# Performance work log

Hardware: AMD Instinct MI355X
Metric: run time of the kernel (lower is better)

## Reference

```python
import jax, jax.numpy as jnp
import numpy as np

# 9 jitter shifts: (L, R, T, B) padding applied to `input`; `target` gets the
# opposite padding (L<->R, T<->B swapped), producing a 1-pixel relative shift.
SHIFTS = ((0, 0, 0, 0), (0, 0, 1, 0), (0, 0, 0, 1), (1, 0, 0, 0), (0, 1, 0, 0),
          (1, 0, 1, 0), (0, 1, 0, 1), (0, 1, 1, 0), (1, 0, 0, 1))
SMIN_K = 32.0


def _shifted_diff(inp, tgt, L, R, T, B):
    # get_opposite in the original simply swaps the pad pair
    Lt, Rt = R, L
    Tt, Bt = B, T
    # ConstantPad2d((L,R,T,B)) pads last dim by (L,R), second-to-last by (T,B)
    pi = jnp.pad(inp, ((0, 0), (T, B), (L, R)))
    pt = jnp.pad(tgt, ((0, 0), (Tt, Bt), (Lt, Rt)))  # same padded shape
    d = jnp.abs(pi - pt)
    n, m, k = d.shape
    # crop back to the original (batch, max_len, dim) window
    return d[:, T:m - B, L:k - R]


def setup_inputs() -> dict:
    key = jax.random.key(0)
    k1, k2 = jax.random.split(key)
    B, T, D = 64, 2048, 80
    return {
        "input": jax.random.normal(k1, (B, T, D), dtype=jnp.float32),
        "target": jax.random.normal(k2, (B, T, D), dtype=jnp.float32),
    }


def reference(input, target):
    # (batch, max_len, dim, 9): abs-diff for each of the 9 relative shifts
    diffs = jnp.stack(
        [_shifted_diff(input, target, L, R, T, B) for (L, R, T, B) in SHIFTS],
        axis=-1,
    )
    # smooth minimum over the 9 shifts: -log(sum(exp(-k*t)))/k (stable via logsumexp)
    sm = -jax.scipy.special.logsumexp(-SMIN_K * diffs, axis=-1) / SMIN_K
    center = diffs[..., 0]  # unshifted abs-diff
    # average of the center diff and the smooth-min, reduced to a scalar loss
    return 0.5 * (jnp.mean(center) + jnp.mean(sm))
```

## Files before the change

### kernel.cpp

```cpp
#include <hip/hip_runtime.h>
#include <math.h>

#define BATCH 64
#define TLEN 2048
#define DIM 80
#define DQ (DIM / 4)
#define TT 4
#define TCHUNKS (TLEN / TT)
#define THREADS 256
#define NSTRIPS (BATCH * TCHUNKS * DQ)
#define NBLOCKS (NSTRIPS / THREADS)

#define SMIN_C  46.166241308446828f
#define SMIN_RC 0.02166084939249829f


__device__ __forceinline__ void load_row(float r[6], const float* __restrict__ base,
                                         int t, int q) {
    if (t >= 0 && t < TLEN) {
        const float* p = base + (size_t)t * DIM;
        const float4 v = *(const float4*)p;
        r[0] = (q > 0)      ? p[-1] : 0.f;
        r[1] = v.x; r[2] = v.y; r[3] = v.z; r[4] = v.w;
        r[5] = (q < DQ - 1) ? p[4]  : 0.f;
    } else {
#pragma unroll
        for (int i = 0; i < 6; ++i) r[i] = 0.f;
    }
}

__device__ __forceinline__ float elem_loss(float x, const float* rm, const float* r0,
                                           const float* rp, int e) {
    float v[9];
#pragma unroll
    for (int i = 0; i < 3; ++i) {
        v[0 + i] = fabsf(x - rm[e + i]);
        v[3 + i] = fabsf(x - r0[e + i]);
        v[6 + i] = fabsf(x - rp[e + i]);
    }
    const float center = v[4];
    float m = fminf(fminf(fminf(v[0], v[1]), fminf(v[2], v[3])),
                    fminf(fminf(v[4], v[5]), fminf(v[6], v[7])));
    m = fminf(m, v[8]);
    const float cm = SMIN_C * m;
    float S = 0.f;
#pragma unroll
    for (int s = 0; s < 9; ++s)
        S += __builtin_amdgcn_exp2f(fmaf(-SMIN_C, v[s], cm));
    const float sm = m - __builtin_amdgcn_logf(S) * SMIN_RC;
    return center + sm;
}

__global__ __launch_bounds__(THREADS) void jitter_kernel(
    const float* __restrict__ inp, const float* __restrict__ tgt,
    float* __restrict__ ws)
{
    __shared__ float wsum[THREADS / 64];

    const int n   = blockIdx.x * THREADS + threadIdx.x;
    const int q   = n % DQ;
    const int rem = n / DQ;
    const int tc  = rem % TCHUNKS;
    const int b   = rem / TCHUNKS;
    const int t0  = tc * TT;
    const int d0  = q * 4;

    const float* tgb = tgt + (size_t)b * TLEN * DIM + d0;
    const float* inb = inp + (size_t)b * TLEN * DIM + d0;

    float rm[6], r0[6], rp[6];
    load_row(rm, tgb, t0 - 1, q);
    load_row(r0, tgb, t0,     q);

    float acc = 0.f;
#pragma unroll
    for (int lt = 0; lt < TT; ++lt) {
        load_row(rp, tgb, t0 + lt + 1, q);
        const float4 in4 = *(const float4*)(inb + (size_t)(t0 + lt) * DIM);
        acc += elem_loss(in4.x, rm, r0, rp, 0);
        acc += elem_loss(in4.y, rm, r0, rp, 1);
        acc += elem_loss(in4.z, rm, r0, rp, 2);
        acc += elem_loss(in4.w, rm, r0, rp, 3);
#pragma unroll
        for (int i = 0; i < 6; ++i) { rm[i] = r0[i]; r0[i] = rp[i]; }
    }

#pragma unroll
    for (int off = 32; off > 0; off >>= 1)
        acc += __shfl_down(acc, off, 64);
    const int lane = threadIdx.x & 63, wid = threadIdx.x >> 6;
    if (lane == 0) wsum[wid] = acc;
    __syncthreads();
    if (threadIdx.x == 0) {
        float tot = 0.f;
#pragma unroll
        for (int w = 0; w < THREADS / 64; ++w) tot += wsum[w];
        ws[blockIdx.x] = tot;
    }
}

__global__ __launch_bounds__(256) void reduce_kernel(const float* __restrict__ ws,
                                                     float* __restrict__ out) {
    __shared__ float wsum[4];
    float s = 0.f;
    for (int i = threadIdx.x; i < NBLOCKS; i += 256) s += ws[i];
#pragma unroll
    for (int off = 32; off > 0; off >>= 1)
        s += __shfl_down(s, off, 64);
    const int lane = threadIdx.x & 63, wid = threadIdx.x >> 6;
    if (lane == 0) wsum[wid] = s;
    __syncthreads();
    if (threadIdx.x == 0) {
        float tot = wsum[0] + wsum[1] + wsum[2] + wsum[3];
        out[0] = tot * (0.5f / (float)((size_t)BATCH * TLEN * DIM));
    }
}

extern "C" void kernel_launch(void* const* d_in, const int* in_sizes, int n_in,
                              void* d_out, int out_size, void* d_ws, size_t ws_size,
                              hipStream_t stream) {
    const float* inp = (const float*)d_in[0];
    const float* tgt = (const float*)d_in[1];
    float* ws  = (float*)d_ws;
    float* out = (float*)d_out;

    jitter_kernel<<<NBLOCKS, THREADS, 0, stream>>>(inp, tgt, ws);
    reduce_kernel<<<1, 256, 0, stream>>>(ws, out);
}
```

Measured before the change: 112.5 us.

## Stage target tile with halo rows in shared memory per block

```diff
diff --git a/kernel.cpp b/kernel.cpp
--- a/kernel.cpp
+++ b/kernel.cpp
@@ -5,29 +5,15 @@
 #define TLEN 2048
 #define DIM 80
 #define DQ (DIM / 4)
+#define TCH 64
+#define NCH (TLEN / TCH)
 #define TT 4
-#define TCHUNKS (TLEN / TT)
-#define THREADS 256
-#define NSTRIPS (BATCH * TCHUNKS * DQ)
-#define NBLOCKS (NSTRIPS / THREADS)
+#define THREADS 320
+#define NBLOCKS (BATCH * NCH)
 
 #define SMIN_C  46.166241308446828f
 #define SMIN_RC 0.02166084939249829f
 
-
-__device__ __forceinline__ void load_row(float r[6], const float* __restrict__ base,
-                                         int t, int q) {
-    if (t >= 0 && t < TLEN) {
-        const float* p = base + (size_t)t * DIM;
-        const float4 v = *(const float4*)p;
-        r[0] = (q > 0)      ? p[-1] : 0.f;
-        r[1] = v.x; r[2] = v.y; r[3] = v.z; r[4] = v.w;
-        r[5] = (q < DQ - 1) ? p[4]  : 0.f;
-    } else {
-#pragma unroll
-        for (int i = 0; i < 6; ++i) r[i] = 0.f;
-    }
-}
 
 __device__ __forceinline__ float elem_loss(float x, const float* rm, const float* r0,
                                            const float* rp, int e) {
@@ -39,44 +25,73 @@
         v[6 + i] = fabsf(x - rp[e + i]);
     }
     const float center = v[4];
-    float m = fminf(fminf(fminf(v[0], v[1]), fminf(v[2], v[3])),
-                    fminf(fminf(v[4], v[5]), fminf(v[6], v[7])));
-    m = fminf(m, v[8]);
+    const float m0 = fminf(fminf(v[0], v[1]), v[2]);
+    const float m1 = fminf(fminf(v[3], v[4]), v[5]);
+    const float m2 = fminf(fminf(v[6], v[7]), v[8]);
+    const float m  = fminf(fminf(m0, m1), m2);
     const float cm = SMIN_C * m;
-    float S = 0.f;
+    float ex[9];
 #pragma unroll
     for (int s = 0; s < 9; ++s)
-        S += __builtin_amdgcn_exp2f(fmaf(-SMIN_C, v[s], cm));
-    const float sm = m - __builtin_amdgcn_logf(S) * SMIN_RC;
-    return center + sm;
+        ex[s] = __builtin_amdgcn_exp2f(fmaf(-SMIN_C, v[s], cm));
+    const float S = ((ex[0] + ex[1]) + (ex[2] + ex[3]))
+                  + (((ex[4] + ex[5]) + (ex[6] + ex[7])) + ex[8]);
+    return center + m - __builtin_amdgcn_logf(S) * SMIN_RC;
 }
 
 __global__ __launch_bounds__(THREADS) void jitter_kernel(
     const float* __restrict__ inp, const float* __restrict__ tgt,
     float* __restrict__ ws)
 {
+    __shared__ __align__(16) float sm[(TCH + 2) * DIM];
     __shared__ float wsum[THREADS / 64];
 
-    const int n   = blockIdx.x * THREADS + threadIdx.x;
-    const int q   = n % DQ;
-    const int rem = n / DQ;
-    const int tc  = rem % TCHUNKS;
-    const int b   = rem / TCHUNKS;
-    const int t0  = tc * TT;
-    const int d0  = q * 4;
+    const int tc  = blockIdx.x & (NCH - 1);
+    const int b   = blockIdx.x >> 5;
+    const int t0  = tc * TCH;
+    const int tid = threadIdx.x;
 
-    const float* tgb = tgt + (size_t)b * TLEN * DIM + d0;
-    const float* inb = inp + (size_t)b * TLEN * DIM + d0;
+    const int sr = (tc == 0)       ? 1   : 0;
+    const int er = (tc == NCH - 1) ? TCH : TCH + 1;
+    const int nf = (er - sr + 1) * DIM;
+    const float* gsrc = tgt + ((size_t)b * TLEN + (t0 - 1 + sr)) * DIM;
+    float* sdst = sm + sr * DIM;
+    for (int i = tid * 4; i < nf; i += THREADS * 4)
+        *(float4*)(sdst + i) = *(const float4*)(gsrc + i);
+    if (tc == 0 && tid < DIM / 4)
+        *(float4*)(sm + tid * 4) = make_float4(0.f, 0.f, 0.f, 0.f);
+    if (tc == NCH - 1 && tid < DIM / 4)
+        *(float4*)(sm + (TCH + 1) * DIM + tid * 4) = make_float4(0.f, 0.f, 0.f, 0.f);
+    __syncthreads();
+
+    const int q  = tid % DQ;
+    const int rs = tid / DQ;
+    const int d0 = q * 4;
+
+    const float* inb = inp + ((size_t)b * TLEN + t0 + rs * TT) * DIM + d0;
 
     float rm[6], r0[6], rp[6];
-    load_row(rm, tgb, t0 - 1, q);
-    load_row(r0, tgb, t0,     q);
+    {
+        const float* p0 = sm + (rs * TT) * DIM + d0;
+        const float* p1 = p0 + DIM;
+        rm[0] = (q > 0) ? p0[-1] : 0.f;
+        rm[1] = p0[0]; rm[2] = p0[1]; rm[3] = p0[2]; rm[4] = p0[3];
+        rm[5] = (q < DQ - 1) ? p0[4] : 0.f;
+        r0[0] = (q > 0) ? p1[-1] : 0.f;
+        r0[1] = p1[0]; r0[2] = p1[1]; r0[3] = p1[2]; r0[4] = p1[3];
+        r0[5] = (q < DQ - 1) ? p1[4] : 0.f;
+    }
 
     float acc = 0.f;
 #pragma unroll
     for (int lt = 0; lt < TT; ++lt) {
-        load_row(rp, tgb, t0 + lt + 1, q);
-        const float4 in4 = *(const float4*)(inb + (size_t)(t0 + lt) * DIM);
+        const float* pp = sm + (rs * TT + lt + 2) * DIM + d0;
+        rp[0] = (q > 0) ? pp[-1] : 0.f;
+        const float4 v = *(const float4*)pp;
+        rp[1] = v.x; rp[2] = v.y; rp[3] = v.z; rp[4] = v.w;
+        rp[5] = (q < DQ - 1) ? pp[4] : 0.f;
+
+        const float4 in4 = *(const float4*)(inb + (size_t)lt * DIM);
         acc += elem_loss(in4.x, rm, r0, rp, 0);
         acc += elem_loss(in4.y, rm, r0, rp, 1);
         acc += elem_loss(in4.z, rm, r0, rp, 2);
@@ -88,10 +103,10 @@
 #pragma unroll
     for (int off = 32; off > 0; off >>= 1)
         acc += __shfl_down(acc, off, 64);
-    const int lane = threadIdx.x & 63, wid = threadIdx.x >> 6;
+    const int lane = tid & 63, wid = tid >> 6;
     if (lane == 0) wsum[wid] = acc;
     __syncthreads();
-    if (threadIdx.x == 0) {
+    if (tid == 0) {
         float tot = 0.f;
 #pragma unroll
         for (int w = 0; w < THREADS / 64; ++w) tot += wsum[w];
```

After: 114.2 us. No clear change (+1.5%).
